# Optimization experiments

Hardware: AMD Instinct MI355X
Metric: run time of the kernel (lower is better)

## Reference

```python
import jax, jax.numpy as jnp
import numpy as np

N = 50000
E = 1600000
IN_F = 512
OUT_F = 128
NEG_SLOPE = 0.01   # nn.LeakyReLU() default
TEMPERATURE = 0.5


def setup_inputs() -> dict:
    key = jax.random.key(0)
    k1, k2, k3, k4 = jax.random.split(key, 4)
    h = jax.random.normal(k1, (N, IN_F), dtype=jnp.float32)
    # xavier_uniform with gain=1.414
    limW = 1.414 * np.sqrt(6.0 / (IN_F + OUT_F))
    W = jax.random.uniform(k2, (IN_F, OUT_F), minval=-limW, maxval=limW, dtype=jnp.float32)
    lima = 1.414 * np.sqrt(6.0 / (2 * OUT_F + 1))
    a = jax.random.uniform(k3, (2 * OUT_F, 1), minval=-lima, maxval=lima, dtype=jnp.float32)
    edge_index = jax.random.randint(k4, (2, E), 0, N, dtype=jnp.int64)
    return {"h": h, "W": W, "a": a, "edge_index": edge_index}


def reference(h, W, a, edge_index):
    # Inference: F.dropout(training=False) is identity.
    Wh = h @ W                                   # [N, F_out]
    src = edge_index[0]                          # row indices -> softmax segments
    dst = edge_index[1]
    # cat([Wh[src], Wh[dst]]) @ a == (Wh @ a1)[src] + (Wh @ a2)[dst]
    a1 = a[:OUT_F, 0]
    a2 = a[OUT_F:, 0]
    s1 = Wh @ a1                                 # [N]
    s2 = Wh @ a2                                 # [N]
    e = s1[src] + s2[dst]                        # [E]
    e = jnp.where(e >= 0, e, NEG_SLOPE * e)      # LeakyReLU
    logits = e / TEMPERATURE
    # sparse softmax over dim=1 (per source-node row segments)
    seg_max = jax.ops.segment_max(logits, src, num_segments=N)  # [N]
    ex = jnp.exp(logits - seg_max[src])          # [E]
    denom = jax.ops.segment_sum(ex, src, num_segments=N)        # [N]
    att = ex / denom[src]                        # [E]
    # sparse-dense matmul: h_prime[i] = sum_j att(i,j) * Wh[j]
    h_prime = jax.ops.segment_sum(att[:, None] * Wh[dst], src, num_segments=N)  # [N, F_out]
    return jax.nn.relu(h_prime)                  # concat=True path
```

## Files before the change

### kernel.cpp

```cpp
#include <hip/hip_runtime.h>
#include <cstdint>
#include <cstddef>

#define N_NODES 50000
#define N_EDGES 1600000
#define IN_FEAT 512
#define OUT_FEAT 128
#define NEG_SLOPE 0.01f
#define INV_TEMP 2.0f
#define PAD_DEG 128

#define BUCKETS 400
#define BNODES 125
#define BCAP 5000
#define A_BLOCKS 250
#define A_EPC (N_EDGES / A_BLOCKS)
#define A_G4 (A_EPC / 4)

typedef __attribute__((ext_vector_type(8))) short short8;
typedef __attribute__((ext_vector_type(4))) float f32x4;

#define GLOBAL_AS __attribute__((address_space(1)))
#define LDS_AS __attribute__((address_space(3)))

__device__ inline unsigned short f2bf(float x) {
    unsigned int u = __float_as_uint(x);
    unsigned int r = (u + 0x7fffu + ((u >> 16) & 1u)) >> 16;
    return (unsigned short)r;
}
__device__ inline float bf2f(unsigned short b) {
    return __uint_as_float(((unsigned int)b) << 16);
}


__global__ __launch_bounds__(256) void binA_kernel(const int* __restrict__ src,
                                                   const int* __restrict__ dst,
                                                   int* __restrict__ bucket_cursor,
                                                   int* __restrict__ binned) {
    __shared__ int cntL[BUCKETS];
    __shared__ int baseL[BUCKETS];
    int t = threadIdx.x;
    for (int i = t; i < BUCKETS; i += 256) cntL[i] = 0;
    __syncthreads();
    size_t ebase = (size_t)blockIdx.x * A_EPC;

    for (int g = t; g < A_G4; g += 256) {
        int4 s4 = *(const int4*)(src + ebase + (size_t)g * 4);
#pragma unroll
        for (int j = 0; j < 4; ++j) {
            int s = (&s4.x)[j];
            atomicAdd(&cntL[s / BNODES], 1);
        }
    }
    __syncthreads();
    for (int i = t; i < BUCKETS; i += 256) {
        int c = cntL[i];
        baseL[i] = c ? atomicAdd(&bucket_cursor[i], c) : 0;
        cntL[i] = 0;
    }
    __syncthreads();
    for (int g = t; g < A_G4; g += 256) {
        int4 s4 = *(const int4*)(src + ebase + (size_t)g * 4);
        int4 d4 = *(const int4*)(dst + ebase + (size_t)g * 4);
#pragma unroll
        for (int j = 0; j < 4; ++j) {
            int s = (&s4.x)[j];
            int b = s / BNODES;
            int sl = s - b * BNODES;
            int pos = atomicAdd(&cntL[b], 1);
            int slot = baseL[b] + pos;
            if (slot < BCAP)
                binned[(size_t)b * BCAP + slot] = (sl << 16) | (&d4.x)[j];
        }
    }
}


__global__ __launch_bounds__(256) void binB_kernel(const int* __restrict__ bucket_cursor,
                                                   const int* __restrict__ binned,
                                                   int* __restrict__ cnt,
                                                   int* __restrict__ csr) {
    __shared__ int cL[BNODES];
    int b = blockIdx.x;
    int t = threadIdx.x;
    if (t < BNODES) cL[t] = 0;
    __syncthreads();
    int m = min(bucket_cursor[b], BCAP);
    const int* bp = binned + (size_t)b * BCAP;
    int n0 = b * BNODES;
    for (int i = t; i < m; i += 256) {
        int p = bp[i];
        int sl = p >> 16;
        int d = p & 0xFFFF;
        int pos = atomicAdd(&cL[sl], 1);
        if (pos < PAD_DEG) csr[(size_t)(n0 + sl) * PAD_DEG + pos] = d;
    }
    __syncthreads();
    if (t < BNODES) cnt[n0 + t] = min(cL[t], PAD_DEG);
}

__global__ __launch_bounds__(256) void convert_w_kernel(const float* __restrict__ W,
                                                        unsigned short* __restrict__ Wt,
                                                        int* __restrict__ bucket_cursor) {
    int tid = blockIdx.x * blockDim.x + threadIdx.x;
    if (tid < BUCKETS) bucket_cursor[tid] = 0;
    if (tid >= IN_FEAT * OUT_FEAT) return;
    int n = tid >> 9;
    int k = tid & 511;
    Wt[tid] = f2bf(W[k * OUT_FEAT + n]);
}


__global__ __launch_bounds__(256) void mfma_gemm_kernel(const float* __restrict__ h,
                                                        const unsigned short* __restrict__ Wt,
                                                        const float* __restrict__ a_vec,
                                                        unsigned short* __restrict__ Whb,
                                                        float* __restrict__ s1,
                                                        float* __restrict__ s2) {
    __shared__ unsigned short lA[4 * 2 * 64 * 8];
    __shared__ unsigned short lB[8 * 2 * 64 * 8];

    int t = threadIdx.x;
    int w = t >> 6;
    int L = t & 63;
    int m0 = blockIdx.x * 64;

    int arow = m0 + w * 16 + (L & 15);
    bool arow_ok = arow < N_NODES;
    int kq = (L >> 4) * 8;

    f32x4 acc[8];
#pragma unroll
    for (int i = 0; i < 8; ++i) acc[i] = (f32x4){0.f, 0.f, 0.f, 0.f};

    for (int k0 = 0; k0 < IN_FEAT; k0 += 64) {
        float4 av[2][2];
#pragma unroll
        for (int c = 0; c < 2; ++c) {
            av[c][0] = make_float4(0.f, 0.f, 0.f, 0.f);
            av[c][1] = make_float4(0.f, 0.f, 0.f, 0.f);
        }
        if (arow_ok) {
            const float* arp = h + (size_t)arow * IN_FEAT + k0 + kq;
            av[0][0] = *(const float4*)(arp);
            av[0][1] = *(const float4*)(arp + 4);
            av[1][0] = *(const float4*)(arp + 32);
            av[1][1] = *(const float4*)(arp + 36);
        }
#pragma unroll
        for (int c = 0; c < 4; ++c) {
            int nb = w * 2 + (c >> 1);
            int ksub = c & 1;
            const GLOBAL_AS unsigned short* g =
                (const GLOBAL_AS unsigned short*)(Wt + (size_t)(nb * 16 + (L & 15)) * IN_FEAT +
                                                  (k0 + ksub * 32 + kq));
            LDS_AS unsigned short* lp = (LDS_AS unsigned short*)(lB + (nb * 2 + ksub) * 512);
            __builtin_amdgcn_global_load_lds((const GLOBAL_AS void*)g, (LDS_AS void*)lp, 16, 0, 0);
        }
#pragma unroll
        for (int c = 0; c < 2; ++c) {
            short8 v;
            v[0] = (short)f2bf(av[c][0].x); v[1] = (short)f2bf(av[c][0].y);
            v[2] = (short)f2bf(av[c][0].z); v[3] = (short)f2bf(av[c][0].w);
            v[4] = (short)f2bf(av[c][1].x); v[5] = (short)f2bf(av[c][1].y);
            v[6] = (short)f2bf(av[c][1].z); v[7] = (short)f2bf(av[c][1].w);
            *(short8*)(lA + ((w * 2 + c) * 64 + L) * 8) = v;
        }
        __syncthreads();
#pragma unroll
        for (int ksub = 0; ksub < 2; ++ksub) {
            short8 af = *(const short8*)(lA + ((w * 2 + ksub) * 64 + L) * 8);
#pragma unroll
            for (int nb = 0; nb < 8; ++nb) {
                short8 bf = *(const short8*)(lB + ((nb * 2 + ksub) * 64 + L) * 8);
                acc[nb] = __builtin_amdgcn_mfma_f32_16x16x32_bf16(af, bf, acc[nb], 0, 0, 0);
            }
        }
        __syncthreads();
    }

    int col0 = L & 15;
    int rbase = m0 + w * 16 + (L >> 4) * 4;

    float a1c[8], a2c[8];
#pragma unroll
    for (int nb = 0; nb < 8; ++nb) {
        a1c[nb] = a_vec[nb * 16 + col0];
        a2c[nb] = a_vec[128 + nb * 16 + col0];
    }

#pragma unroll
    for (int r = 0; r < 4; ++r) {
        int row = rbase + r;
        bool ok = row < N_NODES;
        float p1 = 0.f, p2 = 0.f;
        if (ok) {
            unsigned short* orow = Whb + (size_t)row * OUT_FEAT;
#pragma unroll
            for (int nb = 0; nb < 8; ++nb) {
                float v = acc[nb][r];
                orow[nb * 16 + col0] = f2bf(v);
                p1 = fmaf(v, a1c[nb], p1);
                p2 = fmaf(v, a2c[nb], p2);
            }
        }
#pragma unroll
        for (int off = 8; off > 0; off >>= 1) {
            p1 += __shfl_xor(p1, off, 64);
            p2 += __shfl_xor(p2, off, 64);
        }
        if (ok && col0 == 0) {
            s1[row] = p1;
            s2[row] = p2;
        }
    }
}


__global__ __launch_bounds__(256) void node_kernel(const unsigned short* __restrict__ Whb,
                                                   const float* __restrict__ s1,
                                                   const float* __restrict__ s2,
                                                   const int* __restrict__ cnt,
                                                   const int* __restrict__ csr,
                                                   float* __restrict__ out) {
    int lane = threadIdx.x & 63;
    int w = threadIdx.x >> 6;
    int n = blockIdx.x * 4 + w;
    if (n >= N_NODES) return;
    int deg = cnt[n];
    size_t start = (size_t)n * PAD_DEG;
    int g = lane >> 4;
    int fo = lane & 15;

    float accv[8];
#pragma unroll
    for (int f = 0; f < 8; ++f) accv[f] = 0.f;
    float inv = 0.f;

    if (deg > 0) {
        float s1n = s1[n];
        int d0 = 0, d1 = 0;
        float ex0 = 0.f, ex1 = 0.f;
        if (lane < deg) {
            d0 = csr[start + lane];
            float ev = s1n + s2[d0];
            ev = ev >= 0.f ? ev : NEG_SLOPE * ev;
            ex0 = __expf(ev * INV_TEMP);
        }
        if (lane + 64 < deg) {
            d1 = csr[start + lane + 64];
            float ev = s1n + s2[d1];
            ev = ev >= 0.f ? ev : NEG_SLOPE * ev;
            ex1 = __expf(ev * INV_TEMP);
        }
        float denom = ex0 + ex1;
#pragma unroll
        for (int off = 32; off > 0; off >>= 1) denom += __shfl_xor(denom, off, 64);
        inv = 1.0f / denom;

#pragma unroll 2
        for (int jj = 0; jj < deg; jj += 4) {
            int e = jj + g;
            bool hi = jj >= 64;
            float exs = hi ? ex1 : ex0;
            int dsel = hi ? d1 : d0;
            float p = __shfl(exs, e & 63, 64);
            int dd = __shfl(dsel, e & 63, 64);
            short8 row = *(const short8*)(Whb + (size_t)dd * OUT_FEAT + fo * 8);
#pragma unroll
            for (int f = 0; f < 8; ++f)
                accv[f] = fmaf(p, bf2f((unsigned short)row[f]), accv[f]);
        }
#pragma unroll
        for (int f = 0; f < 8; ++f) {
            accv[f] += __shfl_xor(accv[f], 16, 64);
            accv[f] += __shfl_xor(accv[f], 32, 64);
        }
    }

    if (g == 0) {
        float* orow = out + (size_t)n * OUT_FEAT + fo * 8;
        float4 o0, o1;
        o0.x = fmaxf(accv[0] * inv, 0.f); o0.y = fmaxf(accv[1] * inv, 0.f);
        o0.z = fmaxf(accv[2] * inv, 0.f); o0.w = fmaxf(accv[3] * inv, 0.f);
        o1.x = fmaxf(accv[4] * inv, 0.f); o1.y = fmaxf(accv[5] * inv, 0.f);
        o1.z = fmaxf(accv[6] * inv, 0.f); o1.w = fmaxf(accv[7] * inv, 0.f);
        *(float4*)(orow) = o0;
        *(float4*)(orow + 4) = o1;
    }
}


extern "C" void kernel_launch(void* const* d_in, const int* in_sizes, int n_in,
                              void* d_out, int out_size, void* d_ws, size_t ws_size,
                              hipStream_t stream) {
    const float* h = (const float*)d_in[0];
    const float* W = (const float*)d_in[1];
    const float* a = (const float*)d_in[2];
    const int* edge = (const int*)d_in[3];
    const int* src = edge;
    const int* dst = edge + N_EDGES;
    float* out = (float*)d_out;

    char* ws = (char*)d_ws;
    size_t off = 0;
    auto alloc = [&](size_t bytes) -> void* {
        void* p = ws + off;
        off = (off + bytes + 255) & ~(size_t)255;
        return p;
    };
    unsigned short* Whb = (unsigned short*)alloc((size_t)N_NODES * OUT_FEAT * sizeof(unsigned short));
    float* s1 = (float*)alloc((size_t)N_NODES * sizeof(float));
    float* s2 = (float*)alloc((size_t)N_NODES * sizeof(float));
    int* cnt = (int*)alloc((size_t)N_NODES * sizeof(int));
    int* csr = (int*)alloc((size_t)N_NODES * PAD_DEG * sizeof(int));
    unsigned short* Wt = (unsigned short*)alloc((size_t)IN_FEAT * OUT_FEAT * sizeof(unsigned short));
    int* bucket_cursor = (int*)alloc((size_t)BUCKETS * sizeof(int));
    int* binned = (int*)alloc((size_t)BUCKETS * BCAP * sizeof(int));

    convert_w_kernel<<<(IN_FEAT * OUT_FEAT + 255) / 256, 256, 0, stream>>>(W, Wt, bucket_cursor);
    binA_kernel<<<A_BLOCKS, 256, 0, stream>>>(src, dst, bucket_cursor, binned);
    binB_kernel<<<BUCKETS, 256, 0, stream>>>(bucket_cursor, binned, cnt, csr);
    mfma_gemm_kernel<<<(N_NODES + 63) / 64, 256, 0, stream>>>(h, Wt, a, Whb, s1, s2);
    node_kernel<<<(N_NODES + 3) / 4, 256, 0, stream>>>(Whb, s1, s2, cnt, csr, out);
}
```

Before: 270.0 us.

## Double-buffer W tiles in LDS and keep A fragments in registers

Restructures the GEMM k-loop into a software pipeline. The next W tile is loaded asynchronously into a second LDS buffer and the next h fragment is prefetched into registers while the current tile is being multiplied. The A operand no longer round-trips through LDS, because each lane already holds its own fragment, which also removes one barrier per iteration. The cost is doubled LDS for B and more registers for the prefetched fragments, which may lower occupancy. The GEMM is only one part of a larger multi-kernel pipeline.

```diff
diff --git a/kernel.cpp b/kernel.cpp
--- a/kernel.cpp
+++ b/kernel.cpp
@@ -117,8 +117,7 @@
                                                         unsigned short* __restrict__ Whb,
                                                         float* __restrict__ s1,
                                                         float* __restrict__ s2) {
-    __shared__ unsigned short lA[4 * 2 * 64 * 8];
-    __shared__ unsigned short lB[8 * 2 * 64 * 8];
+    __shared__ unsigned short lB[2][8 * 2 * 64 * 8];
 
     int t = threadIdx.x;
     int w = t >> 6;
@@ -128,25 +127,13 @@
     int arow = m0 + w * 16 + (L & 15);
     bool arow_ok = arow < N_NODES;
     int kq = (L >> 4) * 8;
+    const float* arp = h + (size_t)arow * IN_FEAT + kq;
 
     f32x4 acc[8];
 #pragma unroll
     for (int i = 0; i < 8; ++i) acc[i] = (f32x4){0.f, 0.f, 0.f, 0.f};
 
-    for (int k0 = 0; k0 < IN_FEAT; k0 += 64) {
-        float4 av[2][2];
-#pragma unroll
-        for (int c = 0; c < 2; ++c) {
-            av[c][0] = make_float4(0.f, 0.f, 0.f, 0.f);
-            av[c][1] = make_float4(0.f, 0.f, 0.f, 0.f);
-        }
-        if (arow_ok) {
-            const float* arp = h + (size_t)arow * IN_FEAT + k0 + kq;
-            av[0][0] = *(const float4*)(arp);
-            av[0][1] = *(const float4*)(arp + 4);
-            av[1][0] = *(const float4*)(arp + 32);
-            av[1][1] = *(const float4*)(arp + 36);
-        }
+    auto stageB = [&](int buf, int k0) {
 #pragma unroll
         for (int c = 0; c < 4; ++c) {
             int nb = w * 2 + (c >> 1);
@@ -154,9 +141,47 @@
             const GLOBAL_AS unsigned short* g =
                 (const GLOBAL_AS unsigned short*)(Wt + (size_t)(nb * 16 + (L & 15)) * IN_FEAT +
                                                   (k0 + ksub * 32 + kq));
-            LDS_AS unsigned short* lp = (LDS_AS unsigned short*)(lB + (nb * 2 + ksub) * 512);
+            LDS_AS unsigned short* lp = (LDS_AS unsigned short*)(&lB[buf][(nb * 2 + ksub) * 512]);
             __builtin_amdgcn_global_load_lds((const GLOBAL_AS void*)g, (LDS_AS void*)lp, 16, 0, 0);
         }
+    };
+
+    float4 av[2][2];
+#pragma unroll
+    for (int c = 0; c < 2; ++c) {
+        av[c][0] = make_float4(0.f, 0.f, 0.f, 0.f);
+        av[c][1] = make_float4(0.f, 0.f, 0.f, 0.f);
+    }
+    if (arow_ok) {
+        av[0][0] = *(const float4*)(arp);
+        av[0][1] = *(const float4*)(arp + 4);
+        av[1][0] = *(const float4*)(arp + 32);
+        av[1][1] = *(const float4*)(arp + 36);
+    }
+    stageB(0, 0);
+    __syncthreads();
+
+#pragma unroll
+    for (int it = 0; it < 8; ++it) {
+        const int buf = it & 1;
+
+        if (it < 7) stageB(buf ^ 1, (it + 1) * 64);
+
+        float4 avn[2][2];
+#pragma unroll
+        for (int c = 0; c < 2; ++c) {
+            avn[c][0] = make_float4(0.f, 0.f, 0.f, 0.f);
+            avn[c][1] = make_float4(0.f, 0.f, 0.f, 0.f);
+        }
+        if (it < 7 && arow_ok) {
+            const float* p = arp + (it + 1) * 64;
+            avn[0][0] = *(const float4*)(p);
+            avn[0][1] = *(const float4*)(p + 4);
+            avn[1][0] = *(const float4*)(p + 32);
+            avn[1][1] = *(const float4*)(p + 36);
+        }
+
+        short8 af[2];
 #pragma unroll
         for (int c = 0; c < 2; ++c) {
             short8 v;
@@ -164,19 +189,24 @@
             v[2] = (short)f2bf(av[c][0].z); v[3] = (short)f2bf(av[c][0].w);
             v[4] = (short)f2bf(av[c][1].x); v[5] = (short)f2bf(av[c][1].y);
             v[6] = (short)f2bf(av[c][1].z); v[7] = (short)f2bf(av[c][1].w);
-            *(short8*)(lA + ((w * 2 + c) * 64 + L) * 8) = v;
-        }
+            af[c] = v;
+        }
+
+#pragma unroll
+        for (int ksub = 0; ksub < 2; ++ksub) {
+#pragma unroll
+            for (int nb = 0; nb < 8; ++nb) {
+                short8 bf = *(const short8*)(&lB[buf][((nb * 2 + ksub) * 64 + L) * 8]);
+                acc[nb] = __builtin_amdgcn_mfma_f32_16x16x32_bf16(af[ksub], bf, acc[nb], 0, 0, 0);
+            }
+        }
+
         __syncthreads();
 #pragma unroll
-        for (int ksub = 0; ksub < 2; ++ksub) {
-            short8 af = *(const short8*)(lA + ((w * 2 + ksub) * 64 + L) * 8);
-#pragma unroll
-            for (int nb = 0; nb < 8; ++nb) {
-                short8 bf = *(const short8*)(lB + ((nb * 2 + ksub) * 64 + L) * 8);
-                acc[nb] = __builtin_amdgcn_mfma_f32_16x16x32_bf16(af, bf, acc[nb], 0, 0, 0);
-            }
-        }
-        __syncthreads();
+        for (int c = 0; c < 2; ++c) {
+            av[c][0] = avn[c][0];
+            av[c][1] = avn[c][1];
+        }
     }
 
     int col0 = L & 15;
```

Result: no change. 267.3 us (-1.0%).
